# Kernel tuning notes

Measured on AMD Instinct MI355X. Metric: run time of the kernel, lower is better.

## Reference

```python
import jax, jax.numpy as jnp
import numpy as np

B, S, H, NH = 8, 1042, 768, 12
HD = H // NH            # 64
P = 1024                # patch tokens (32x32 grid); RoPE applied to last P tokens
MLP = 2048              # int(768 * 8/3)
EPS = 1e-6


def _rope_tables():
    # mirrors precompute_rope_freqs_2d(HD, P): inside, dim = HD//2 = 32
    dim = HD // 2
    t = int(P ** 0.5)  # 32
    freqs = 1.0 / (10000.0 ** (np.arange(0, dim, 2, dtype=np.float32) / dim))  # (16,)
    pos = np.arange(t, dtype=np.float32)
    fh = pos[:, None] * freqs[None, :]                       # (t,16)
    f = np.concatenate([np.tile(fh[:, None, :], (1, t, 1)),
                        np.tile(fh[None, :, :], (t, 1, 1))], axis=-1)  # (t,t,32)
    f = f.reshape(P, dim)                                    # (1024,32)
    return jnp.asarray(np.cos(f)), jnp.asarray(np.sin(f))


def setup_inputs() -> dict:
    key = jax.random.key(0)
    ks = jax.random.split(key, 20)
    r = lambda k, sh, sc: (jax.random.normal(k, sh, jnp.float32) * sc)
    cos, sin = _rope_tables()
    return {
        "x": jax.random.normal(ks[0], (B, S, H), jnp.float32),
        "rope_cos": cos, "rope_sin": sin,
        "Wq": r(ks[1], (H, H), 0.02), "Wk": r(ks[2], (H, H), 0.02),
        "Wv": r(ks[3], (H, H), 0.02), "Wo": r(ks[4], (H, H), 0.02),
        "q_norm_w": jnp.ones((HD,), jnp.float32),
        "k_norm_w": jnp.ones((HD,), jnp.float32),
        "gate_W": r(ks[5], (H, NH), 0.02),
        "gate_b": jnp.full((NH,), 4.0, jnp.float32),
        "norm1_w": jnp.ones((H,), jnp.float32),
        "norm2_w": jnp.ones((H,), jnp.float32),
        "W_gate": r(ks[6], (H, MLP), 0.02),
        "W_up": r(ks[7], (H, MLP), 0.02),
        "W_down": r(ks[8], (MLP, H), 0.02),
        "attn_scale": r(ks[9], (H,), 0.1),   # zero-init in module; randn for nontrivial grads
        "mlp_scale": r(ks[10], (H,), 0.1),
    }


def _rmsnorm(x, w):
    return x * jax.lax.rsqrt(jnp.mean(x * x, axis=-1, keepdims=True) + EPS) * w


def _apply_rope(x, cos, sin):
    # x: (B,S,NH,HD); rotate only the last P (patch) tokens, consecutive-pair complex rotation
    xp = x[:, -P:].reshape(B, P, NH, HD // 2, 2)
    x0, x1 = xp[..., 0], xp[..., 1]
    c = cos[None, :, None, :]
    s = sin[None, :, None, :]
    rot = jnp.stack([x0 * c - x1 * s, x0 * s + x1 * c], axis=-1).reshape(B, P, NH, HD)
    return jnp.concatenate([x[:, :-P], rot], axis=1)


def reference(x, rope_cos, rope_sin, Wq, Wk, Wv, Wo, q_norm_w, k_norm_w,
              gate_W, gate_b, norm1_w, norm2_w, W_gate, W_up, W_down,
              attn_scale, mlp_scale):
    # --- attention branch (QwenGatedRoPEAttention) ---
    h = _rmsnorm(x, norm1_w)
    q = (h @ Wq).reshape(B, S, NH, HD)
    k = (h @ Wk).reshape(B, S, NH, HD)
    v = (h @ Wv).reshape(B, S, NH, HD)
    q = _rmsnorm(q, q_norm_w)
    k = _rmsnorm(k, k_norm_w)
    q = _apply_rope(q, rope_cos, rope_sin)
    k = _apply_rope(k, rope_cos, rope_sin)
    q = q / jnp.sqrt(jnp.asarray(HD, jnp.float32))
    scores = jnp.einsum('bqhd,bkhd->bhqk', q, k)          # (B,NH,S,S)
    probs = jax.nn.softmax(scores.astype(jnp.float32), axis=-1)
    attn = jnp.einsum('bhqk,bkhd->bqhd', probs, v)        # (B,S,NH,HD)
    gate = jax.nn.sigmoid((h @ gate_W)[..., None] + gate_b[None, None, :, None])
    attn = (attn * gate).reshape(B, S, H)
    x = x + (attn @ Wo) * attn_scale
    # --- SwiGLU MLP branch ---
    h2 = _rmsnorm(x, norm2_w)
    mlp = (jax.nn.silu(h2 @ W_gate) * (h2 @ W_up)) @ W_down
    x = x + mlp * mlp_scale
    return x
```

## Files before the change

kernel.cpp:

```cpp
#include <hip/hip_runtime.h>
#include <hip/hip_bf16.h>
#include <stdint.h>

#define B_   8
#define S_   1042
#define H_   768
#define NH_  12
#define HD_  64
#define MLP_ 2048
#define T_   (B_*S_)
#define MP_  8448
#define SP_  1088
#define EPS_ 1e-6f
#define PSLICE ((long)96 * SP_ * 64)

typedef __attribute__((ext_vector_type(8))) short bf16x8v;
typedef __attribute__((ext_vector_type(4))) float f32x4;
typedef __hip_bfloat16 bf16;

typedef __attribute__((address_space(1))) const void gas_void;
typedef __attribute__((address_space(3))) void las_void;

__device__ inline void gload_lds16(const void* g, void* l) {
  __builtin_amdgcn_global_load_lds((gas_void*)g, (las_void*)l, 16, 0, 0);
}

#define BARRIER asm volatile("s_barrier" ::: "memory")
#define VMCNT2  asm volatile("s_waitcnt vmcnt(2)" ::: "memory")
#define VMCNT0  asm volatile("s_waitcnt vmcnt(0)" ::: "memory")

__global__ __launch_bounds__(256) void wcvt_t(const float* __restrict__ W, bf16* __restrict__ o,
                                              int K, int N) {
  __shared__ float tile[32][33];
  int kt = blockIdx.x, nt = blockIdx.y;
  int t = threadIdx.x;
  int r = t >> 5, c = t & 31;
#pragma unroll
  for (int i = 0; i < 4; i++)
    tile[i * 8 + r][c] = W[(long)(kt * 32 + i * 8 + r) * N + nt * 32 + c];
  __syncthreads();
#pragma unroll
  for (int i = 0; i < 4; i++)
    o[(long)(nt * 32 + i * 8 + r) * K + kt * 32 + c] = __float2bfloat16(tile[c][i * 8 + r]);
}

__global__ __launch_bounds__(256) void wcvt_gu(const float* __restrict__ Wg,
                                               const float* __restrict__ Wu,
                                               bf16* __restrict__ o) {
  __shared__ float tile[32][33];
  int kt = blockIdx.x, nt = blockIdx.y;
  int t = threadIdx.x;
  int r = t >> 5, c = t & 31;
  const float* src = (c < 16) ? Wg : Wu;
  int col = nt * 16 + (c & 15);
#pragma unroll
  for (int i = 0; i < 4; i++)
    tile[i * 8 + r][c] = src[(long)(kt * 32 + i * 8 + r) * MLP_ + col];
  __syncthreads();
#pragma unroll
  for (int i = 0; i < 4; i++)
    o[(long)(nt * 32 + i * 8 + r) * 768 + kt * 32 + c] = __float2bfloat16(tile[c][i * 8 + r]);
}

template <int GATE>
__global__ __launch_bounds__(256) void rmsnorm_k(const float* __restrict__ x,
                                                 const float* __restrict__ w,
                                                 bf16* __restrict__ o,
                                                 const float* __restrict__ gW,
                                                 const float* __restrict__ gb,
                                                 float* __restrict__ gate, int Mreal) {
  int row = blockIdx.x;
  bf16* orow = o + (long)row * H_;
  int t = threadIdx.x;
  if (row >= Mreal) {
    for (int i = t; i < H_; i += 256) orow[i] = __float2bfloat16(0.f);
    return;
  }
  const float* xr = x + (long)row * H_;
  float v0 = xr[t], v1 = xr[t + 256], v2 = xr[t + 512];
  float s = v0 * v0 + v1 * v1 + v2 * v2;
  for (int off = 32; off; off >>= 1) s += __shfl_down(s, off);
  __shared__ float red[4];
  __shared__ float gred[4][12];
  if ((t & 63) == 0) red[t >> 6] = s;
  __syncthreads();
  float tot = red[0] + red[1] + red[2] + red[3];
  float inv = rsqrtf(tot * (1.f / H_) + EPS_);
  float h0 = v0 * inv * w[t], h1 = v1 * inv * w[t + 256], h2 = v2 * inv * w[t + 512];
  orow[t]       = __float2bfloat16(h0);
  orow[t + 256] = __float2bfloat16(h1);
  orow[t + 512] = __float2bfloat16(h2);
  if (GATE) {
    const float* g0 = gW + (long)t * 12;
    const float* g1 = gW + (long)(t + 256) * 12;
    const float* g2 = gW + (long)(t + 512) * 12;
    float g[12];
#pragma unroll
    for (int n = 0; n < 12; n++) g[n] = h0 * g0[n] + h1 * g1[n] + h2 * g2[n];
#pragma unroll
    for (int n = 0; n < 12; n++) {
      float v = g[n];
      v += __shfl_xor(v, 1); v += __shfl_xor(v, 2); v += __shfl_xor(v, 4);
      v += __shfl_xor(v, 8); v += __shfl_xor(v, 16); v += __shfl_xor(v, 32);
      if ((t & 63) == 0) gred[t >> 6][n] = v;
    }
    __syncthreads();
    if (t < 12) {
      float s4 = gred[0][t] + gred[1][t] + gred[2][t] + gred[3][t];
      gate[(long)row * 12 + t] = 1.f / (1.f + __expf(-(s4 + gb[t])));
    }
  }
}

template <int EPI, int KT, int LD, int NKS>
__global__ __launch_bounds__(512) void gemm256(
    const bf16* __restrict__ A, const bf16* __restrict__ Bt, void* __restrict__ Out,
    const float* __restrict__ resid, const float* __restrict__ scale,
    int N, int nbn, int Mreal, bf16* __restrict__ alt3) {
  __shared__ __align__(16) bf16 lds[2][4][128 * 32];
  int tid = threadIdx.x;
  int lane = tid & 63, wid = tid >> 6;
  int wr = wid >> 2, wc = wid & 3;
  int lr = lane & 15, lg = lane >> 4;

  int nwg = gridDim.x;
  int bid = blockIdx.x;
  int q = nwg >> 3, r8 = nwg & 7;
  int xcd = bid & 7, idx = bid >> 3;
  int wg = (xcd < r8 ? xcd * (q + 1) : r8 * (q + 1) + (xcd - r8) * q) + idx;

  int ks = 0;
  if (NKS > 1) {
    int bps = nwg / NKS;
    ks = wg / bps;
    wg = wg - ks * bps;
    A += (long)ks * KT * 32;
    Bt += (long)ks * KT * 32;
  }
  int bm = wg / nbn, bn = wg - bm * nbn;

  const bf16 *aP[2], *bP[2];
  {
    int off = lr * 32 + ((lg ^ ((lr >> 1) & 3)) * 8);
#pragma unroll
    for (int b = 0; b < 2; b++) {
      aP[b] = &lds[b][wr][off];
      bP[b] = &lds[b][2 + (wc >> 1)][(wc & 1) * 2048 + off];
    }
  }
  int srow = tid >> 2;
  int cc = (tid & 3) ^ ((srow >> 1) & 3);
  const bf16 *aB[2], *bB[2];
#pragma unroll
  for (int h = 0; h < 2; h++) {
    aB[h] = A + ((long)bm * 256 + h * 128 + srow) * LD + cc * 8;
    bB[h] = Bt + ((long)bn * 256 + h * 128 + srow) * LD + cc * 8;
  }

#define STA(buf, half, kt) gload_lds16(aB[half] + (kt) * 32, &lds[buf][half][tid * 8]);
#define STB(buf, half, kt) gload_lds16(bB[half] + (kt) * 32, &lds[buf][2 + (half)][tid * 8]);

  f32x4 z; z[0] = z[1] = z[2] = z[3] = 0.f;
  f32x4 acc[8][4];
#pragma unroll
  for (int mi = 0; mi < 8; mi++)
#pragma unroll
    for (int ni = 0; ni < 4; ni++) acc[mi][ni] = z;

  bf16x8v bf[4];
  bf16x8v af[2];

  STA(0, 0, 0); STA(0, 1, 0); STB(0, 0, 0); STB(0, 1, 0);
  STB(1, 0, 1); STB(1, 1, 1);
  VMCNT2;
  BARRIER;

#define PHASE(p, bb, STG, VM)                                                   \
  {                                                                             \
    if ((p) == 0) {                                                             \
      _Pragma("unroll") for (int ni = 0; ni < 4; ni++)                          \
        bf[ni] = *(const bf16x8v*)(bP[bb] + ni * 512);                          \
    }                                                                           \
    af[0] = *(const bf16x8v*)(aP[bb] + (2 * (p)) * 512);                        \
    af[1] = *(const bf16x8v*)(aP[bb] + (2 * (p) + 1) * 512);                    \
    STG;                                                                        \
    BARRIER;                                                                    \
    __builtin_amdgcn_s_setprio(1);                                              \
    _Pragma("unroll") for (int dm = 0; dm < 2; dm++)                            \
      _Pragma("unroll") for (int ni = 0; ni < 4; ni++)                          \
        acc[2 * (p) + dm][ni] = __builtin_amdgcn_mfma_f32_16x16x32_bf16(        \
            af[dm], bf[ni], acc[2 * (p) + dm][ni], 0, 0, 0);                    \
    __builtin_amdgcn_s_setprio(0);                                              \
    if (VM) VMCNT2;                                                             \
  }

#define ITERBODY(i)                                                             \
  {                                                                             \
    int u = 2 * (i) + 1;                                                        \
    int t2 = (2 * (i) + 2 < KT) ? 2 * (i) + 2 : KT - 1;                         \
    int t3 = (2 * (i) + 3 < KT) ? 2 * (i) + 3 : KT - 1;                         \
    PHASE(0, 0, STA(1, 0, u), 0);                                               \
    PHASE(1, 0, STA(1, 1, u), 0);                                               \
    PHASE(2, 0, STB(0, 0, t2), 0);                                              \
    PHASE(3, 0, STB(0, 1, t2), 1);                                              \
    PHASE(0, 1, STA(0, 0, t2), 0);                                              \
    PHASE(1, 1, STA(0, 1, t2), 0);                                              \
    PHASE(2, 1, STB(1, 0, t3), 0);                                              \
    PHASE(3, 1, STB(1, 1, t3), 1);                                              \
  }

  if (KT <= 12) {
#pragma unroll
    for (int i = 0; i < KT / 2; i++) ITERBODY(i);
  } else {
#pragma unroll 2
    for (int i = 0; i < KT / 2; i++) ITERBODY(i);
  }
  VMCNT0;
#undef ITERBODY
#undef PHASE
#undef STA
#undef STB

  long rowbase = (long)bm * 256 + wr * 128;
  int colbase = bn * 256 + wc * 64;
  if (EPI == 0) {
    bf16* O;
    if (NKS > 1) O = (ks < 3) ? (bf16*)Out + (long)ks * PSLICE : alt3;
    else O = (bf16*)Out;
#pragma unroll
    for (int mi = 0; mi < 8; mi++)
#pragma unroll
      for (int ni = 0; ni < 4; ni++)
#pragma unroll
        for (int r = 0; r < 4; r++)
          O[(rowbase + mi * 16 + lg * 4 + r) * N + colbase + ni * 16 + lr] =
              __float2bfloat16(acc[mi][ni][r]);
  } else if (EPI == 1) {
    float* O = (float*)Out;
#pragma unroll
    for (int ni = 0; ni < 4; ni++) {
      float sc = scale[colbase + ni * 16 + lr];
#pragma unroll
      for (int mi = 0; mi < 8; mi++)
#pragma unroll
        for (int r = 0; r < 4; r++) {
          long row = rowbase + mi * 16 + lg * 4 + r;
          long col = colbase + ni * 16 + lr;
          if (row < Mreal)
            O[row * N + col] = resid[row * N + col] + acc[mi][ni][r] * sc;
        }
    }
  } else {
    bf16* O = (bf16*)Out;
    int oc0 = colbase >> 1;
#pragma unroll
    for (int mi = 0; mi < 8; mi++)
#pragma unroll
      for (int p = 0; p < 2; p++)
#pragma unroll
        for (int r = 0; r < 4; r++) {
          float g = acc[mi][2 * p][r], u = acc[mi][2 * p + 1][r];
          float v = g / (1.f + __expf(-g)) * u;
          O[(rowbase + mi * 16 + lg * 4 + r) * 2048 + oc0 + p * 16 + lr] =
              __float2bfloat16(v);
        }
  }
}

__global__ __launch_bounds__(256) void mlp2_reduce(
    const bf16* __restrict__ p012, const bf16* __restrict__ p3,
    const float* __restrict__ x2, const float* __restrict__ mscale,
    float* __restrict__ out) {
  long i = (long)blockIdx.x * 256 + threadIdx.x;
  long row = i / 96;
  int c8 = (int)(i - row * 96) * 8;
  long off = row * 768 + c8;
  float a[8];
#pragma unroll
  for (int j = 0; j < 8; j++) a[j] = 0.f;
#pragma unroll
  for (int s = 0; s < 3; s++) {
    bf16x8v v = *(const bf16x8v*)(p012 + s * PSLICE + off);
#pragma unroll
    for (int j = 0; j < 8; j++) {
      short sv = v[j];
      a[j] += __bfloat162float(*reinterpret_cast<bf16*>(&sv));
    }
  }
  {
    bf16x8v v = *(const bf16x8v*)(p3 + off);
#pragma unroll
    for (int j = 0; j < 8; j++) {
      short sv = v[j];
      a[j] += __bfloat162float(*reinterpret_cast<bf16*>(&sv));
    }
  }
#pragma unroll
  for (int j = 0; j < 8; j++)
    out[off + j] = x2[off + j] + a[j] * mscale[c8 + j];
}

__global__ __launch_bounds__(256) void vtran(const bf16* __restrict__ qkv, bf16* __restrict__ vtf) {
  __shared__ bf16 tile[32][66];
  int st = blockIdx.x, bh = blockIdx.y;
  int bb = bh / NH_, h = bh - bb * NH_;
  int s0 = st * 32;
  int t = threadIdx.x;
  int si = t >> 6, d = t & 63;
#pragma unroll
  for (int i = 0; i < 8; i++) {
    int s = s0 + i * 4 + si;
    bf16 v = __float2bfloat16(0.f);
    if (s < S_) v = qkv[(long)(bb * S_ + s) * 2304 + 1536 + h * 64 + d];
    tile[i * 4 + si][d] = v;
  }
  __syncthreads();
  int dd = t >> 5, sj = t & 31;
#pragma unroll
  for (int i = 0; i < 8; i++) {
    int d2 = i * 8 + dd;
    vtf[((long)bh * 64 + d2) * SP_ + s0 + sj] = tile[sj][d2];
  }
}

__global__ __launch_bounds__(768) void qkv_post(
    const bf16* __restrict__ qkv, const float* __restrict__ qw, const float* __restrict__ kw,
    const float* __restrict__ cosT, const float* __restrict__ sinT,
    bf16* __restrict__ qf, bf16* __restrict__ kf) {
  int tok = blockIdx.x;
  int bb = tok / S_, s = tok - bb * S_;
  int h = threadIdx.x >> 6, d = threadIdx.x & 63;
  const bf16* base = qkv + (long)tok * 2304 + h * 64 + d;
  float q = __bfloat162float(base[0]);
  float k = __bfloat162float(base[768]);
  float qs = q * q, ks = k * k;
  for (int off = 32; off; off >>= 1) {
    qs += __shfl_xor(qs, off);
    ks += __shfl_xor(ks, off);
  }
  q *= rsqrtf(qs * (1.f / 64.f) + EPS_) * qw[d];
  k *= rsqrtf(ks * (1.f / 64.f) + EPS_) * kw[d];
  if (s >= S_ - 1024) {
    int pos = s - (S_ - 1024);
    int i = d >> 1;
    float c = cosT[pos * 32 + i], sn = sinT[pos * 32 + i];
    float qp = __shfl_xor(q, 1), kp = __shfl_xor(k, 1);
    if (d & 1) { q = qp * sn + q * c; k = kp * sn + k * c; }
    else       { q = q * c - qp * sn; k = k * c - kp * sn; }
  }
  q *= 0.125f * 1.44269504088896f;
  long o1 = ((long)(bb * NH_ + h) * SP_ + s) * 64 + d;
  qf[o1] = __float2bfloat16(q);
  kf[o1] = __float2bfloat16(k);
}

#define SWZ(row, cc) (((row) << 6) + ((((cc) ^ ((row) & 7))) << 3))

__global__ __launch_bounds__(256) void attn_k(
    const bf16* __restrict__ qf, const bf16* __restrict__ kf, const bf16* __restrict__ vtf,
    const float* __restrict__ gate, bf16* __restrict__ attn_g) {
  __shared__ __align__(16) bf16 Ks[2][64 * 64];
  __shared__ __align__(16) bf16 Vs[2][64 * 64];
  int bid = blockIdx.x;
  int w = (bid & 7) * 204 + (bid >> 3);
  int bh = w / 17, qb = w - bh * 17;
  int bb = bh / NH_, h = bh - bb * NH_;
  int tid = threadIdx.x;
  int lane = tid & 63, wv = tid >> 6;
  int lr = lane & 15, lg = lane >> 4;
  const bf16* qbase = qf + (long)bh * SP_ * 64;
  const bf16* kbase = kf + (long)bh * SP_ * 64;
  const bf16* vbase = vtf + (long)bh * 64 * SP_;

  int q_l = qb * 64 + wv * 16 + lr;
  bf16x8v qB0 = *(const bf16x8v*)(qbase + (long)q_l * 64 + lg * 8);
  bf16x8v qB1 = *(const bf16x8v*)(qbase + (long)q_l * 64 + 32 + lg * 8);

  f32x4 z; z[0] = z[1] = z[2] = z[3] = 0.f;
  f32x4 acc[4] = {z, z, z, z};
  float tsacc = 0.f;

  auto stage = [&](int buf, int kidx) {
#pragma unroll
    for (int inst = 0; inst < 2; inst++) {
      int c = inst * 256 + tid;
      int row = c >> 3, slot = c & 7;
      int cc = slot ^ (row & 7);
      gload_lds16(kbase + (long)(kidx + row) * 64 + cc * 8, &Ks[buf][c * 8]);
    }
#pragma unroll
    for (int inst = 0; inst < 2; inst++) {
      int c = inst * 256 + tid;
      int row = c >> 3, slot = c & 7;
      int cc = slot ^ (row & 7);
      gload_lds16(vbase + (long)row * SP_ + kidx + cc * 8, &Vs[buf][c * 8]);
    }
  };

  stage(0, 0);
  VMCNT0;
  __syncthreads();
  int cur = 0;

  for (int kt = 0; kt < SP_ / 64; kt++) {
    int kidx = kt * 64;
    if (kt < SP_ / 64 - 1) stage(cur ^ 1, kidx + 64);

    f32x4 p[4];
    __builtin_amdgcn_s_setprio(1);
#pragma unroll
    for (int mt = 0; mt < 4; mt++) {
      int row = mt * 16 + lr;
      bf16x8v k0 = *(const bf16x8v*)&Ks[cur][SWZ(row, lg)];
      bf16x8v k1 = *(const bf16x8v*)&Ks[cur][SWZ(row, lg + 4)];
      f32x4 t = z;
      t = __builtin_amdgcn_mfma_f32_16x16x32_bf16(k0, qB0, t, 0, 0, 0);
      t = __builtin_amdgcn_mfma_f32_16x16x32_bf16(k1, qB1, t, 0, 0, 0);
      p[mt] = t;
    }
    __builtin_amdgcn_s_setprio(0);

    if (kidx + 64 > S_) {
#pragma unroll
      for (int mt = 0; mt < 4; mt++)
#pragma unroll
        for (int r = 0; r < 4; r++)
          if (kidx + mt * 16 + lg * 4 + r >= S_) p[mt][r] = -1e30f;
    }

#pragma unroll
    for (int mt = 0; mt < 4; mt++)
#pragma unroll
      for (int r = 0; r < 4; r++) {
        float e = exp2f(p[mt][r]);
        p[mt][r] = e;
        tsacc += e;
      }

    uint32_t w0[4], w1[4];
#pragma unroll
    for (int mt = 0; mt < 4; mt++) {
      asm("v_cvt_pk_bf16_f32 %0, %1, %2" : "=v"(w0[mt]) : "v"(p[mt][0]), "v"(p[mt][1]));
      asm("v_cvt_pk_bf16_f32 %0, %1, %2" : "=v"(w1[mt]) : "v"(p[mt][2]), "v"(p[mt][3]));
    }
    bf16x8v aP[2];
#pragma unroll
    for (int t2 = 0; t2 < 2; t2++) {
      union { uint32_t u[4]; bf16x8v v; } cvt;
#pragma unroll
      for (int wd = 0; wd < 4; wd++) {
        uint32_t a = (wd & 1) ? w1[2 * t2] : w0[2 * t2];
        uint32_t b = (wd & 1) ? w1[2 * t2 + 1] : w0[2 * t2 + 1];
        uint32_t val = (lg & 2) ? b : a;
        int src = ((lg & 1) * 2 + (wd >> 1)) * 16 + lr;
        cvt.u[wd] = (uint32_t)__shfl((int)val, src);
      }
      aP[t2] = cvt.v;
    }
    __builtin_amdgcn_s_setprio(1);
#pragma unroll
    for (int t2 = 0; t2 < 2; t2++)
#pragma unroll
      for (int dt = 0; dt < 4; dt++) {
        int row = dt * 16 + lr;
        bf16x8v vB = *(const bf16x8v*)&Vs[cur][SWZ(row, t2 * 4 + lg)];
        acc[dt] = __builtin_amdgcn_mfma_f32_16x16x32_bf16(aP[t2], vB, acc[dt], 0, 0, 0);
      }
    __builtin_amdgcn_s_setprio(0);

    VMCNT0;
    __syncthreads();
    cur ^= 1;
  }

  tsacc += __shfl_xor(tsacc, 16);
  tsacc += __shfl_xor(tsacc, 32);
  float norm = 0.f;
  if (q_l < S_) norm = gate[((long)bb * S_ + q_l) * 12 + h] / tsacc;
  float nr[4];
#pragma unroll
  for (int r = 0; r < 4; r++) nr[r] = __shfl(norm, lg * 4 + r);
#pragma unroll
  for (int dt = 0; dt < 4; dt++)
#pragma unroll
    for (int r = 0; r < 4; r++) {
      int qr = qb * 64 + wv * 16 + lg * 4 + r;
      if (qr < S_)
        attn_g[((long)bb * S_ + qr) * H_ + h * 64 + dt * 16 + lr] =
            __float2bfloat16(acc[dt][r] * nr[r]);
    }
}

extern "C" void kernel_launch(void* const* d_in, const int* in_sizes, int n_in,
                              void* d_out, int out_size, void* d_ws, size_t ws_size,
                              hipStream_t stream) {
  const float* x    = (const float*)d_in[0];
  const float* cosT = (const float*)d_in[1];
  const float* sinT = (const float*)d_in[2];
  const float* Wq   = (const float*)d_in[3];
  const float* Wk   = (const float*)d_in[4];
  const float* Wv   = (const float*)d_in[5];
  const float* Wo   = (const float*)d_in[6];
  const float* qnw  = (const float*)d_in[7];
  const float* knw  = (const float*)d_in[8];
  const float* gW   = (const float*)d_in[9];
  const float* gb   = (const float*)d_in[10];
  const float* n1w  = (const float*)d_in[11];
  const float* n2w  = (const float*)d_in[12];
  const float* Wg   = (const float*)d_in[13];
  const float* Wu   = (const float*)d_in[14];
  const float* Wd   = (const float*)d_in[15];
  const float* ascale = (const float*)d_in[16];
  const float* mscale = (const float*)d_in[17];

  char* ws = (char*)d_ws;
  size_t off = 0;
  auto alloc = [&](size_t bytes) {
    char* p = ws + off;
    off += (bytes + 255) & ~(size_t)255;
    return p;
  };
  bf16* h_pad  = (bf16*)alloc((size_t)MP_ * H_ * 2);
  bf16* wqkv_t = (bf16*)alloc((size_t)2304 * 768 * 2);
  bf16* wo_t   = (bf16*)alloc((size_t)768 * 768 * 2);
  bf16* wgu_t  = (bf16*)alloc((size_t)4096 * 768 * 2);
  bf16* wdn_t  = (bf16*)alloc((size_t)768 * 2048 * 2);
  bf16* qkv    = (bf16*)alloc((size_t)MP_ * 2304 * 2);
  bf16* qfb    = (bf16*)alloc((size_t)PSLICE * 2);
  bf16* kfb    = (bf16*)alloc((size_t)PSLICE * 2);
  bf16* vtfb   = (bf16*)alloc((size_t)PSLICE * 2);
  float* gateb = (float*)alloc((size_t)T_ * 12 * 4);
  bf16* attn_g = (bf16*)alloc((size_t)MP_ * H_ * 2);
  float* x2    = (float*)alloc((size_t)T_ * H_ * 4);
  bf16* mlpin  = qkv;

  auto wc = [&](const float* W, bf16* o, int K, int N) {
    wcvt_t<<<dim3(K / 32, N / 32), 256, 0, stream>>>(W, o, K, N);
  };
  wc(Wq, wqkv_t, 768, 768);
  wc(Wk, wqkv_t + 768 * 768, 768, 768);
  wc(Wv, wqkv_t + 2 * 768 * 768, 768, 768);
  wc(Wo, wo_t, 768, 768);
  wc(Wd, wdn_t, 2048, 768);
  wcvt_gu<<<dim3(24, 128), 256, 0, stream>>>(Wg, Wu, wgu_t);

  rmsnorm_k<1><<<MP_, 256, 0, stream>>>(x, n1w, h_pad, gW, gb, gateb, T_);

  gemm256<0, 24, 768, 1><<<9 * 33, 512, 0, stream>>>(h_pad, wqkv_t, qkv, nullptr, nullptr,
                                                     2304, 9, MP_, nullptr);

  qkv_post<<<T_, 768, 0, stream>>>(qkv, qnw, knw, cosT, sinT, qfb, kfb);
  vtran<<<dim3(33, 96), 256, 0, stream>>>(qkv, vtfb);

  attn_k<<<1632, 256, 0, stream>>>(qfb, kfb, vtfb, gateb, attn_g);

  gemm256<1, 24, 768, 1><<<3 * 33, 512, 0, stream>>>(attn_g, wo_t, x2, x, ascale,
                                                     768, 3, T_, nullptr);

  rmsnorm_k<0><<<MP_, 256, 0, stream>>>(x2, n2w, h_pad, nullptr, nullptr, nullptr, T_);

  gemm256<2, 24, 768, 1><<<16 * 33, 512, 0, stream>>>(h_pad, wgu_t, mlpin, nullptr, nullptr,
                                                      4096, 16, MP_, nullptr);

  gemm256<0, 16, 2048, 4><<<4 * 3 * 33, 512, 0, stream>>>(mlpin, wdn_t, qfb, nullptr, nullptr,
                                                          768, 3, MP_, attn_g);
  mlp2_reduce<<<(T_ * 96) / 256, 256, 0, stream>>>(qfb, attn_g, x2, mscale, (float*)d_out);
}
```

Baseline: 392.6 us.

## Shrink GEMM tile to 256x128 with 4 waves to double workgroup count

Reworks the gemm256 kernel from a 256x256 tile with 8 waves to a 256x128 tile with 4 waves (256 threads). LDS shrinks to 3 slabs per buffer and the staging pattern is reorganised so each thread issues two loads per A/B half. The B loads now happen once per four phases. All GEMM launches double their grids to cover the narrower N tiles. The aim is more workgroups for better CU fill and lower LDS use per block, at the cost of less B-tile reuse and more global traffic for A.

Result: slower. 438.9 us (+11.8%).

```diff
diff --git a/kernel.cpp b/kernel.cpp
--- a/kernel.cpp
+++ b/kernel.cpp
@@ -113,14 +113,14 @@
 }
 
 template <int EPI, int KT, int LD, int NKS>
-__global__ __launch_bounds__(512) void gemm256(
+__global__ __launch_bounds__(256) void gemm256(
     const bf16* __restrict__ A, const bf16* __restrict__ Bt, void* __restrict__ Out,
     const float* __restrict__ resid, const float* __restrict__ scale,
     int N, int nbn, int Mreal, bf16* __restrict__ alt3) {
-  __shared__ __align__(16) bf16 lds[2][4][128 * 32];
+  __shared__ __align__(16) bf16 lds[2][3][128 * 32];
   int tid = threadIdx.x;
   int lane = tid & 63, wid = tid >> 6;
-  int wr = wid >> 2, wc = wid & 3;
+  int wr = wid >> 1, wc = wid & 1;
   int lr = lane & 15, lg = lane >> 4;
 
   int nwg = gridDim.x;
@@ -145,20 +145,31 @@
 #pragma unroll
     for (int b = 0; b < 2; b++) {
       aP[b] = &lds[b][wr][off];
-      bP[b] = &lds[b][2 + (wc >> 1)][(wc & 1) * 2048 + off];
+      bP[b] = &lds[b][2][wc * 2048 + off];
     }
   }
   int srow = tid >> 2;
   int cc = (tid & 3) ^ ((srow >> 1) & 3);
-  const bf16 *aB[2], *bB[2];
-#pragma unroll
-  for (int h = 0; h < 2; h++) {
-    aB[h] = A + ((long)bm * 256 + h * 128 + srow) * LD + cc * 8;
-    bB[h] = Bt + ((long)bn * 256 + h * 128 + srow) * LD + cc * 8;
-  }
-
-#define STA(buf, half, kt) gload_lds16(aB[half] + (kt) * 32, &lds[buf][half][tid * 8]);
-#define STB(buf, half, kt) gload_lds16(bB[half] + (kt) * 32, &lds[buf][2 + (half)][tid * 8]);
+  const bf16 *aB[2][2], *bB[2];
+#pragma unroll
+  for (int h = 0; h < 2; h++)
+#pragma unroll
+    for (int sub = 0; sub < 2; sub++)
+      aB[h][sub] = A + ((long)bm * 256 + h * 128 + sub * 64 + srow) * LD + cc * 8;
+#pragma unroll
+  for (int sub = 0; sub < 2; sub++)
+    bB[sub] = Bt + ((long)bn * 128 + sub * 64 + srow) * LD + cc * 8;
+
+#define STA(buf, h, kt)                                                         \
+  {                                                                             \
+    gload_lds16(aB[h][0] + (kt) * 32, &lds[buf][h][tid * 8]);                   \
+    gload_lds16(aB[h][1] + (kt) * 32, &lds[buf][h][2048 + tid * 8]);            \
+  }
+#define STB(buf, kt)                                                            \
+  {                                                                             \
+    gload_lds16(bB[0] + (kt) * 32, &lds[buf][2][tid * 8]);                      \
+    gload_lds16(bB[1] + (kt) * 32, &lds[buf][2][2048 + tid * 8]);               \
+  }
 
   f32x4 z; z[0] = z[1] = z[2] = z[3] = 0.f;
   f32x4 acc[8][4];
@@ -170,8 +181,8 @@
   bf16x8v bf[4];
   bf16x8v af[2];
 
-  STA(0, 0, 0); STA(0, 1, 0); STB(0, 0, 0); STB(0, 1, 0);
-  STB(1, 0, 1); STB(1, 1, 1);
+  STA(0, 0, 0); STA(0, 1, 0); STB(0, 0);
+  STB(1, 1);
   VMCNT2;
   BARRIER;
 
@@ -201,12 +212,12 @@
     int t3 = (2 * (i) + 3 < KT) ? 2 * (i) + 3 : KT - 1;                         \
     PHASE(0, 0, STA(1, 0, u), 0);                                               \
     PHASE(1, 0, STA(1, 1, u), 0);                                               \
-    PHASE(2, 0, STB(0, 0, t2), 0);                                              \
-    PHASE(3, 0, STB(0, 1, t2), 1);                                              \
+    PHASE(2, 0, STB(0, t2), 0);                                                 \
+    PHASE(3, 0, (void)0, 1);                                                    \
     PHASE(0, 1, STA(0, 0, t2), 0);                                              \
     PHASE(1, 1, STA(0, 1, t2), 0);                                              \
-    PHASE(2, 1, STB(1, 0, t3), 0);                                              \
-    PHASE(3, 1, STB(1, 1, t3), 1);                                              \
+    PHASE(2, 1, STB(1, t3), 0);                                                 \
+    PHASE(3, 1, (void)0, 1);                                                    \
   }
 
   if (KT <= 12) {
@@ -223,7 +234,7 @@
 #undef STB
 
   long rowbase = (long)bm * 256 + wr * 128;
-  int colbase = bn * 256 + wc * 64;
+  int colbase = bn * 128 + wc * 64;
   if (EPI == 0) {
     bf16* O;
     if (NKS > 1) O = (ks < 3) ? (bf16*)Out + (long)ks * PSLICE : alt3;
@@ -547,23 +558,23 @@
 
   rmsnorm_k<1><<<MP_, 256, 0, stream>>>(x, n1w, h_pad, gW, gb, gateb, T_);
 
-  gemm256<0, 24, 768, 1><<<9 * 33, 512, 0, stream>>>(h_pad, wqkv_t, qkv, nullptr, nullptr,
-                                                     2304, 9, MP_, nullptr);
+  gemm256<0, 24, 768, 1><<<33 * 18, 256, 0, stream>>>(h_pad, wqkv_t, qkv, nullptr, nullptr,
+                                                      2304, 18, MP_, nullptr);
 
   qkv_post<<<T_, 768, 0, stream>>>(qkv, qnw, knw, cosT, sinT, qfb, kfb);
   vtran<<<dim3(33, 96), 256, 0, stream>>>(qkv, vtfb);
 
   attn_k<<<1632, 256, 0, stream>>>(qfb, kfb, vtfb, gateb, attn_g);
 
-  gemm256<1, 24, 768, 1><<<3 * 33, 512, 0, stream>>>(attn_g, wo_t, x2, x, ascale,
-                                                     768, 3, T_, nullptr);
+  gemm256<1, 24, 768, 1><<<33 * 6, 256, 0, stream>>>(attn_g, wo_t, x2, x, ascale,
+                                                     768, 6, T_, nullptr);
 
   rmsnorm_k<0><<<MP_, 256, 0, stream>>>(x2, n2w, h_pad, nullptr, nullptr, nullptr, T_);
 
-  gemm256<2, 24, 768, 1><<<16 * 33, 512, 0, stream>>>(h_pad, wgu_t, mlpin, nullptr, nullptr,
-                                                      4096, 16, MP_, nullptr);
-
-  gemm256<0, 16, 2048, 4><<<4 * 3 * 33, 512, 0, stream>>>(mlpin, wdn_t, qfb, nullptr, nullptr,
-                                                          768, 3, MP_, attn_g);
+  gemm256<2, 24, 768, 1><<<33 * 32, 256, 0, stream>>>(h_pad, wgu_t, mlpin, nullptr, nullptr,
+                                                      4096, 32, MP_, nullptr);
+
+  gemm256<0, 16, 2048, 4><<<4 * 33 * 6, 256, 0, stream>>>(mlpin, wdn_t, qfb, nullptr, nullptr,
+                                                          768, 6, MP_, attn_g);
   mlp2_reduce<<<(T_ * 96) / 256, 256, 0, stream>>>(qfb, attn_g, x2, mscale, (float*)d_out);
 }
```

## Add 128x128-tile GEMM for QKV and gate/up projections

Applied to the files above, without the earlier changes.

Introduces a gemm128 kernel with 128x128 tiles, 256 threads and a double-buffered LDS pipeline, and uses it for the QKV and gate/up GEMMs instead of the 256-tile kernel. The smaller tiles give more workgroups (1188 and 2112 instead of 297 and 528), which should fill the GPU's compute units better. In exchange, each tile reuses its operands less. It also adds an extra barrier after the vmcnt wait in the existing gemm256 pipeline, which affects the Wo and down GEMMs that still use it.

Measured after the change: 394.6 us. Within noise of the previous version (+0.5%).

```diff
diff --git a/kernel.cpp b/kernel.cpp
--- a/kernel.cpp
+++ b/kernel.cpp
@@ -191,7 +191,7 @@
         acc[2 * (p) + dm][ni] = __builtin_amdgcn_mfma_f32_16x16x32_bf16(        \
             af[dm], bf[ni], acc[2 * (p) + dm][ni], 0, 0, 0);                    \
     __builtin_amdgcn_s_setprio(0);                                              \
-    if (VM) VMCNT2;                                                             \
+    if (VM) { VMCNT2; BARRIER; }                                                \
   }
 
 #define ITERBODY(i)                                                             \
@@ -256,6 +256,136 @@
     int oc0 = colbase >> 1;
 #pragma unroll
     for (int mi = 0; mi < 8; mi++)
+#pragma unroll
+      for (int p = 0; p < 2; p++)
+#pragma unroll
+        for (int r = 0; r < 4; r++) {
+          float g = acc[mi][2 * p][r], u = acc[mi][2 * p + 1][r];
+          float v = g / (1.f + __expf(-g)) * u;
+          O[(rowbase + mi * 16 + lg * 4 + r) * 2048 + oc0 + p * 16 + lr] =
+              __float2bfloat16(v);
+        }
+  }
+}
+
+template <int EPI, int KT, int LD>
+__global__ __launch_bounds__(256) void gemm128(
+    const bf16* __restrict__ A, const bf16* __restrict__ Bt, void* __restrict__ Out,
+    int N, int nbn) {
+  __shared__ __align__(16) bf16 lds[2][2][128 * 32];
+  int tid = threadIdx.x;
+  int lane = tid & 63, wid = tid >> 6;
+  int wr = wid >> 1, wc = wid & 1;
+  int lr = lane & 15, lg = lane >> 4;
+
+  int nwg = gridDim.x;
+  int bid = blockIdx.x;
+  int q = nwg >> 3, r8 = nwg & 7;
+  int xcd = bid & 7, idx = bid >> 3;
+  int wg = (xcd < r8 ? xcd * (q + 1) : r8 * (q + 1) + (xcd - r8) * q) + idx;
+  int bm = wg / nbn, bn = wg - bm * nbn;
+
+  const bf16 *aP[2], *bP[2];
+  {
+    int off = lr * 32 + ((lg ^ ((lr >> 1) & 3)) * 8);
+#pragma unroll
+    for (int b = 0; b < 2; b++) {
+      aP[b] = &lds[b][0][wr * 2048 + off];
+      bP[b] = &lds[b][1][wc * 2048 + off];
+    }
+  }
+  int srow = tid >> 2;
+  int cc = (tid & 3) ^ ((srow >> 1) & 3);
+  const bf16 *aB[2], *bB[2];
+#pragma unroll
+  for (int sub = 0; sub < 2; sub++) {
+    aB[sub] = A + ((long)bm * 128 + sub * 64 + srow) * LD + cc * 8;
+    bB[sub] = Bt + ((long)bn * 128 + sub * 64 + srow) * LD + cc * 8;
+  }
+
+#define STA(buf, kt)                                                            \
+  {                                                                             \
+    gload_lds16(aB[0] + (kt) * 32, &lds[buf][0][tid * 8]);                      \
+    gload_lds16(aB[1] + (kt) * 32, &lds[buf][0][2048 + tid * 8]);               \
+  }
+#define STB(buf, kt)                                                            \
+  {                                                                             \
+    gload_lds16(bB[0] + (kt) * 32, &lds[buf][1][tid * 8]);                      \
+    gload_lds16(bB[1] + (kt) * 32, &lds[buf][1][2048 + tid * 8]);               \
+  }
+
+  f32x4 z; z[0] = z[1] = z[2] = z[3] = 0.f;
+  f32x4 acc[4][4];
+#pragma unroll
+  for (int mi = 0; mi < 4; mi++)
+#pragma unroll
+    for (int ni = 0; ni < 4; ni++) acc[mi][ni] = z;
+
+  bf16x8v bf[4];
+  bf16x8v af;
+
+  STA(0, 0); STB(0, 0);
+  STB(1, 1);
+  VMCNT2;
+  BARRIER;
+
+#define PHASE(p, bb, STG, VM)                                                   \
+  {                                                                             \
+    if ((p) == 0) {                                                             \
+      _Pragma("unroll") for (int ni = 0; ni < 4; ni++)                          \
+        bf[ni] = *(const bf16x8v*)(bP[bb] + ni * 512);                          \
+    }                                                                           \
+    af = *(const bf16x8v*)(aP[bb] + (p) * 512);                                 \
+    STG;                                                                        \
+    BARRIER;                                                                    \
+    __builtin_amdgcn_s_setprio(1);                                              \
+    _Pragma("unroll") for (int ni = 0; ni < 4; ni++)                            \
+      acc[p][ni] = __builtin_amdgcn_mfma_f32_16x16x32_bf16(                     \
+          af, bf[ni], acc[p][ni], 0, 0, 0);                                     \
+    __builtin_amdgcn_s_setprio(0);                                              \
+    if (VM) { VMCNT2; BARRIER; }                                                \
+  }
+
+#define ITERBODY(i)                                                             \
+  {                                                                             \
+    int u = 2 * (i) + 1;                                                        \
+    int t2 = (2 * (i) + 2 < KT) ? 2 * (i) + 2 : KT - 1;                         \
+    int t3 = (2 * (i) + 3 < KT) ? 2 * (i) + 3 : KT - 1;                         \
+    PHASE(0, 0, STA(1, u), 0);                                                  \
+    PHASE(1, 0, (void)0, 0);                                                    \
+    PHASE(2, 0, STB(0, t2), 0);                                                 \
+    PHASE(3, 0, (void)0, 1);                                                    \
+    PHASE(0, 1, STA(0, t2), 0);                                                 \
+    PHASE(1, 1, (void)0, 0);                                                    \
+    PHASE(2, 1, STB(1, t3), 0);                                                 \
+    PHASE(3, 1, (void)0, 1);                                                    \
+  }
+
+#pragma unroll 2
+  for (int i = 0; i < KT / 2; i++) ITERBODY(i);
+  VMCNT0;
+#undef ITERBODY
+#undef PHASE
+#undef STA
+#undef STB
+
+  long rowbase = (long)bm * 128 + wr * 64;
+  int colbase = bn * 128 + wc * 64;
+  if (EPI == 0) {
+    bf16* O = (bf16*)Out;
+#pragma unroll
+    for (int mi = 0; mi < 4; mi++)
+#pragma unroll
+      for (int ni = 0; ni < 4; ni++)
+#pragma unroll
+        for (int r = 0; r < 4; r++)
+          O[(rowbase + mi * 16 + lg * 4 + r) * N + colbase + ni * 16 + lr] =
+              __float2bfloat16(acc[mi][ni][r]);
+  } else {
+    bf16* O = (bf16*)Out;
+    int oc0 = colbase >> 1;
+#pragma unroll
+    for (int mi = 0; mi < 4; mi++)
 #pragma unroll
       for (int p = 0; p < 2; p++)
 #pragma unroll
@@ -547,8 +677,7 @@
 
   rmsnorm_k<1><<<MP_, 256, 0, stream>>>(x, n1w, h_pad, gW, gb, gateb, T_);
 
-  gemm256<0, 24, 768, 1><<<9 * 33, 512, 0, stream>>>(h_pad, wqkv_t, qkv, nullptr, nullptr,
-                                                     2304, 9, MP_, nullptr);
+  gemm128<0, 24, 768><<<66 * 18, 256, 0, stream>>>(h_pad, wqkv_t, qkv, 2304, 18);
 
   qkv_post<<<T_, 768, 0, stream>>>(qkv, qnw, knw, cosT, sinT, qfb, kfb);
   vtran<<<dim3(33, 96), 256, 0, stream>>>(qkv, vtfb);
@@ -560,8 +689,7 @@
 
   rmsnorm_k<0><<<MP_, 256, 0, stream>>>(x2, n2w, h_pad, nullptr, nullptr, nullptr, T_);
 
-  gemm256<2, 24, 768, 1><<<16 * 33, 512, 0, stream>>>(h_pad, wgu_t, mlpin, nullptr, nullptr,
-                                                      4096, 16, MP_, nullptr);
+  gemm128<2, 24, 768><<<66 * 32, 256, 0, stream>>>(h_pad, wgu_t, mlpin, 4096, 32);
 
   gemm256<0, 16, 2048, 4><<<4 * 3 * 33, 512, 0, stream>>>(mlpin, wdn_t, qfb, nullptr, nullptr,
                                                           768, 3, MP_, attn_g);
```
